# Kernel tuning notes

Measured on AMD Instinct MI355X. Metric: run time of the kernel, lower is better.

The kernel has to match this reference:

```python
import jax, jax.numpy as jnp
import numpy as np

N_NODES = 50000
N_EDGES = 800000
DIM = 128
N_LAYERS = 2          # num_layers - 1 GIN layers
NUM_GRAPHS = 512      # rows of the sparse graph_pool matrix
BN_EPS = 1e-5


def setup_inputs() -> dict:
    key = jax.random.key(0)
    ks = jax.random.split(key, 10)
    x = jax.random.normal(ks[0], (N_NODES, DIM), dtype=jnp.float32)
    edge_src = jax.random.randint(ks[1], (N_EDGES,), 0, N_NODES, dtype=jnp.int32)
    edge_dst = jax.random.randint(ks[2], (N_EDGES,), 0, N_NODES, dtype=jnp.int32)
    edge_weight = jax.random.uniform(ks[3], (N_EDGES,), dtype=jnp.float32)
    graph_ids = jnp.sort(jax.random.randint(ks[4], (N_NODES,), 0, NUM_GRAPHS, dtype=jnp.int32))
    pool_w = jnp.ones((N_NODES,), dtype=jnp.float32)
    scale = 1.0 / np.sqrt(DIM)
    W1 = jax.random.normal(ks[5], (N_LAYERS, DIM, DIM), dtype=jnp.float32) * scale
    b1 = jnp.zeros((N_LAYERS, DIM), dtype=jnp.float32)
    W2 = jax.random.normal(ks[6], (N_LAYERS, DIM, DIM), dtype=jnp.float32) * scale
    b2 = jnp.zeros((N_LAYERS, DIM), dtype=jnp.float32)
    bn_gamma = jnp.ones((N_LAYERS, DIM), dtype=jnp.float32)
    bn_beta = jnp.zeros((N_LAYERS, DIM), dtype=jnp.float32)
    return {"x": x, "edge_src": edge_src, "edge_dst": edge_dst,
            "edge_weight": edge_weight, "graph_ids": graph_ids, "pool_w": pool_w,
            "W1": W1, "b1": b1, "W2": W2, "b2": b2,
            "bn_gamma": bn_gamma, "bn_beta": bn_beta}


def reference(x, edge_src, edge_dst, edge_weight, graph_ids, pool_w,
              W1, b1, W2, b2, bn_gamma, bn_beta):
    h = x
    n = h.shape[0]
    for l in range(N_LAYERS):
        # pooled = adj @ h, adj in COO form: adj[dst, src] = edge_weight
        msg = edge_weight[:, None] * h[edge_src]                    # [E, D] gather
        pooled = jax.ops.segment_sum(msg, edge_dst, num_segments=n) # [N, D] scatter-add
        # 2-linear MLP (num_mlp_layers=2): Linear -> ReLU -> Linear
        hid = jax.nn.relu(pooled @ W1[l] + b1[l])
        z = hid @ W2[l] + b2[l]
        # BatchNorm1d over the node dimension (training-mode batch stats)
        mu = jnp.mean(z, axis=0)
        var = jnp.mean(jnp.square(z - mu), axis=0)
        z = bn_gamma[l] * (z - mu) * jax.lax.rsqrt(var + BN_EPS) + bn_beta[l]
        h = jax.nn.relu(z)
    x_nodes = h
    # pooled_x = graph_pool @ h, graph_pool[g, i] = pool_w[i] for node i in graph g
    pooled_x = jax.ops.segment_sum(pool_w[:, None] * h, graph_ids,
                                   num_segments=NUM_GRAPHS)
    return pooled_x, x_nodes
```

## Files before the change

kernel.cpp:

```cpp
#include <hip/hip_runtime.h>

#define N_NODES    50000
#define N_EDGES    800000
#define DIM        128
#define NUM_GRAPHS 512
#define BN_EPS     1e-5f

#define NBUCK      196
#define TILE       4096
#define MLP_ROWS   128
#define POOL_SPLIT 4

typedef unsigned int u32;
typedef unsigned short u16;
typedef __attribute__((ext_vector_type(8))) short bf16x8;
typedef __attribute__((ext_vector_type(4))) float f32x4;

__device__ __forceinline__ u16 f2bf(float f) {
    u32 u = __float_as_uint(f);
    u += 0x7FFF + ((u >> 16) & 1);
    return (u16)(u >> 16);
}
__device__ __forceinline__ float bf2f(u16 h) {
    return __uint_as_float((u32)h << 16);
}

__global__ __launch_bounds__(256)
void fill_zero2_kernel(float* __restrict__ p1, int n1, float* __restrict__ p2, int n2)
{
    int stride = gridDim.x * blockDim.x;
    for (int i = blockIdx.x * 256 + threadIdx.x; i < n1 + n2; i += stride) {
        if (i < n1) p1[i] = 0.f;
        else        p2[i - n1] = 0.f;
    }
}

__global__ __launch_bounds__(256)
void cvt_bf16_kernel(const float* __restrict__ in, u16* __restrict__ out, long long n4)
{
    long long stride = (long long)gridDim.x * blockDim.x;
    for (long long i = blockIdx.x * 256LL + threadIdx.x; i < n4; i += stride) {
        float4 v = ((const float4*)in)[i];
        ushort4 o;
        o.x = f2bf(v.x); o.y = f2bf(v.y); o.z = f2bf(v.z); o.w = f2bf(v.w);
        ((ushort4*)out)[i] = o;
    }
}

__global__ __launch_bounds__(256)
void cvt_wt_kernel(const float* __restrict__ W1, const float* __restrict__ W2,
                   u16* __restrict__ wt)
{
    int idx = blockIdx.x * 256 + threadIdx.x;
    if (idx >= 4 * 128 * 128) return;
    int m    = idx >> 14;
    int f    = idx & 16383;
    int c    = (f >> 11) & 7;
    int kk   = (f >> 9) & 3;
    int lane = (f >> 3) & 63;
    int e    = f & 7;
    int k = kk * 32 + ((lane >> 4) << 3) + e;
    int j = c * 16 + (lane & 15);
    const float* src = (m & 1) ? W2 : W1;
    src += (m >> 1) * 128 * 128;
    wt[idx] = f2bf(src[k * 128 + j]);
}

__global__ __launch_bounds__(256)
void bucket_hist(const int* __restrict__ dst, int* __restrict__ bucketCnt)
{
    __shared__ int cnt[NBUCK];
    int t = threadIdx.x;
    if (t < NBUCK) cnt[t] = 0;
    __syncthreads();
    int stride = gridDim.x * blockDim.x;
    for (int i = blockIdx.x * 256 + t; i < N_EDGES / 4; i += stride) {
        int4 d = ((const int4*)dst)[i];
        atomicAdd(&cnt[d.x >> 8], 1);
        atomicAdd(&cnt[d.y >> 8], 1);
        atomicAdd(&cnt[d.z >> 8], 1);
        atomicAdd(&cnt[d.w >> 8], 1);
    }
    __syncthreads();
    if (t < NBUCK && cnt[t] > 0) atomicAdd(&bucketCnt[t], cnt[t]);
}

__global__ __launch_bounds__(256)
void bucket_scan(const int* __restrict__ bucketCnt, int* __restrict__ bucketStart,
                 int* __restrict__ gCursor)
{
    __shared__ int s[256];
    int t = threadIdx.x;
    int v = (t < NBUCK) ? bucketCnt[t] : 0;
    s[t] = v;
    __syncthreads();
    for (int off = 1; off < 256; off <<= 1) {
        int x = (t >= off) ? s[t - off] : 0;
        __syncthreads();
        s[t] += x;
        __syncthreads();
    }
    int excl = s[t] - v;
    if (t <= NBUCK) bucketStart[t] = excl;
    if (t < NBUCK)  gCursor[t] = excl;
}

__global__ __launch_bounds__(512)
void partitionA(const int* __restrict__ src, const int* __restrict__ dst,
                const float* __restrict__ ew, int* __restrict__ gCursor,
                uint2* __restrict__ ed2)
{
    __shared__ int cnt[NBUCK];
    __shared__ int off[NBUCK];
    __shared__ int gb[NBUCK];
    __shared__ u32 stg_sw[TILE];
    __shared__ u32 stg_d[TILE];
    __shared__ int scanb[256];

    const int t = threadIdx.x;
    const int base = blockIdx.x * TILE;
    const int tcnt = min(TILE, N_EDGES - base);

    if (t < NBUCK) cnt[t] = 0;
    __syncthreads();

    u32 swv[8], dv[8];
    int rk[8], bk[8];
    #pragma unroll
    for (int j = 0; j < 8; ++j) {
        int e = base + j * 512 + t;
        if (e < N_EDGES) {
            int d = dst[e];
            swv[j] = ((u32)f2bf(ew[e]) << 16) | (u32)src[e];
            dv[j]  = (u32)d;
            bk[j]  = d >> 8;
            rk[j]  = atomicAdd(&cnt[bk[j]], 1);
        } else bk[j] = -1;
    }
    __syncthreads();

    {
        int v = (t < NBUCK) ? cnt[t] : 0;
        if (t < 256) scanb[t] = v;
        __syncthreads();
        for (int o = 1; o < 256; o <<= 1) {
            int x = (t < 256 && t >= o) ? scanb[t - o] : 0;
            __syncthreads();
            if (t < 256) scanb[t] += x;
            __syncthreads();
        }
        if (t < NBUCK) off[t] = scanb[t] - v;
    }
    __syncthreads();

    #pragma unroll
    for (int j = 0; j < 8; ++j) {
        if (bk[j] >= 0) {
            int idx = off[bk[j]] + rk[j];
            stg_sw[idx] = swv[j];
            stg_d[idx]  = dv[j];
        }
    }
    if (t < NBUCK && cnt[t] > 0) gb[t] = atomicAdd(&gCursor[t], cnt[t]);
    __syncthreads();

    for (int j = t; j < tcnt; j += 512) {
        u32 d = stg_d[j];
        int b = (int)(d >> 8);
        int pos = gb[b] + (j - off[b]);
        ed2[pos] = make_uint2(stg_sw[j], d);
    }
}

__global__ __launch_bounds__(256)
void partitionB(const uint2* __restrict__ ed2, const int* __restrict__ bucketStart,
                int* __restrict__ rowptr, u32* __restrict__ ed)
{
    __shared__ int hist[256];
    __shared__ int sc[256];
    __shared__ int cur[256];

    const int b = blockIdx.x;
    const int t = threadIdx.x;
    const int s = bucketStart[b];
    const int n = bucketStart[b + 1] - s;

    hist[t] = 0;
    __syncthreads();
    for (int j = t; j < n; j += 256)
        atomicAdd(&hist[ed2[s + j].y & 255u], 1);
    __syncthreads();

    int v = hist[t];
    sc[t] = v;
    __syncthreads();
    for (int o = 1; o < 256; o <<= 1) {
        int x = (t >= o) ? sc[t - o] : 0;
        __syncthreads();
        sc[t] += x;
        __syncthreads();
    }
    int excl = sc[t] - v;
    rowptr[b * 256 + t] = s + excl;
    cur[t] = s + excl;
    __syncthreads();

    for (int j = t; j < n; j += 256) {
        uint2 r = ed2[s + j];
        int d = (int)(r.y & 255u);
        int p = atomicAdd(&cur[d], 1);
        ed[p] = r.x;
    }
}

template<bool BN>
__global__ __launch_bounds__(256)
void gather_spmm(const u16* __restrict__ h, const u32* __restrict__ ed,
                 const int* __restrict__ rowptr, u16* __restrict__ pooled,
                 const float* __restrict__ stats, const float* __restrict__ gamma,
                 const float* __restrict__ beta)
{
    __shared__ float scs[128];
    __shared__ float shs[128];
    if (BN) {
        if (threadIdx.x < 128) {
            int c = threadIdx.x;
            float mu  = stats[c] * (1.f / N_NODES);
            float var = stats[128 + c] * (1.f / N_NODES) - mu * mu;
            float s   = gamma[c] * rsqrtf(var + BN_EPS);
            scs[c] = s;
            shs[c] = beta[c] - mu * s;
        }
        __syncthreads();
    }

    int node = blockIdx.x * 16 + (threadIdx.x >> 4);
    int lane = threadIdx.x & 15;
    int beg = rowptr[node];
    int end = rowptr[node + 1];

    float sc8[8], sh8[8];
    if (BN) {
        #pragma unroll
        for (int q = 0; q < 8; ++q) {
            sc8[q] = scs[lane * 8 + q];
            sh8[q] = shs[lane * 8 + q];
        }
    }

    float acc[8];
    #pragma unroll
    for (int q = 0; q < 8; ++q) acc[q] = 0.f;

    u32 sw_cur = (beg + lane < end) ? ed[beg + lane] : 0u;
    for (int base = beg; base < end; base += 16) {
        u32 sw_next = (base + 16 + lane < end) ? ed[base + 16 + lane] : 0u;
        int cnt = min(16, end - base);
        #pragma unroll 4
        for (int i = 0; i < cnt; ++i) {
            u32 rec = __shfl(sw_cur, i, 16);
            long long s = (long long)(rec & 0xFFFFu);
            float w = bf2f((u16)(rec >> 16));
            bf16x8 hv = *((const bf16x8*)(h + (s << 7)) + lane);
            #pragma unroll
            for (int q = 0; q < 8; ++q) {
                float v = bf2f((u16)hv[q]);
                if (BN) v = fmaxf(v * sc8[q] + sh8[q], 0.f);
                acc[q] += w * v;
            }
        }
        sw_cur = sw_next;
    }
    bf16x8 o;
    #pragma unroll
    for (int q = 0; q < 8; ++q) o[q] = (short)f2bf(acc[q]);
    *((bf16x8*)(pooled + ((long long)node << 7)) + lane) = o;
}

__global__ __launch_bounds__(512)
void fused_mlp(const u16* __restrict__ A, const u16* __restrict__ wtL,
               const float* __restrict__ b1, const float* __restrict__ b2,
               u16* __restrict__ Z, float* __restrict__ stats)
{
    __shared__ __align__(16) u16 wfrag[32768];
    __shared__ float ssum[128];
    __shared__ float ssq[128];

    const int tid  = threadIdx.x;
    const int lane = tid & 63;
    const int wave = tid >> 6;
    const int l15  = lane & 15;
    const int lk   = lane >> 4;
    const int row0 = blockIdx.x * MLP_ROWS;
    const int wrow = wave * 16;

    #pragma unroll
    for (int i = 0; i < 8; ++i) {
        int idx = tid + i * 512;
        *(bf16x8*)&wfrag[idx * 8] = *(const bf16x8*)(wtL + idx * 8);
    }
    if (tid < 128) { ssum[tid] = 0.f; ssq[tid] = 0.f; }

    bf16x8 afr[4];
    {
        int rg = row0 + wrow + l15;
        bool ok = rg < N_NODES;
        const u16* ap = A + (long long)rg * 128 + lk * 8;
        bf16x8 zero = {};
        #pragma unroll
        for (int kk = 0; kk < 4; ++kk)
            afr[kk] = ok ? *(const bf16x8*)(ap + kk * 32) : zero;
    }
    __syncthreads();

    f32x4 acc1[8];
    #pragma unroll
    for (int c = 0; c < 8; ++c) {
        float bv = b1[c * 16 + l15];
        f32x4 a = {bv, bv, bv, bv};
        #pragma unroll
        for (int kk = 0; kk < 4; ++kk) {
            bf16x8 w = *(bf16x8*)&wfrag[((c * 4 + kk) * 64 + lane) * 8];
            a = __builtin_amdgcn_mfma_f32_16x16x32_bf16(afr[kk], w, a, 0, 0, 0);
        }
        acc1[c] = a;
    }
    __syncthreads();

    #pragma unroll
    for (int c = 0; c < 8; ++c) {
        #pragma unroll
        for (int i = 0; i < 4; ++i) {
            int row = wrow + lk * 4 + i;
            int col = c * 16 + l15;
            wfrag[row * 128 + (col ^ ((row & 15) << 3))] = f2bf(fmaxf(acc1[c][i], 0.f));
        }
    }

    bf16x8 afr2[4];
    {
        int row = wrow + l15;
        #pragma unroll
        for (int kk = 0; kk < 4; ++kk)
            afr2[kk] = *(bf16x8*)&wfrag[row * 128 + ((kk * 32 + lk * 8) ^ ((row & 15) << 3))];
    }

    #pragma unroll
    for (int c = 0; c < 8; ++c) {
        float bv = b2[c * 16 + l15];
        f32x4 a = {bv, bv, bv, bv};
        #pragma unroll
        for (int kk = 0; kk < 4; ++kk) {
            bf16x8 w = *(bf16x8*)&wfrag[16384 + ((c * 4 + kk) * 64 + lane) * 8];
            a = __builtin_amdgcn_mfma_f32_16x16x32_bf16(afr2[kk], w, a, 0, 0, 0);
        }
        float s = 0.f, sq = 0.f;
        #pragma unroll
        for (int i = 0; i < 4; ++i) {
            int row = wrow + lk * 4 + i;
            int rg  = row0 + row;
            float v = a[i];
            bool ok = rg < N_NODES;
            if (ok) { s += v; sq += v * v; }
            wfrag[row * 128 + ((c * 16 + l15) ^ ((row & 15) << 3))] = ok ? f2bf(v) : (u16)0;
        }
        s  += __shfl_xor(s, 16);  s  += __shfl_xor(s, 32);
        sq += __shfl_xor(sq, 16); sq += __shfl_xor(sq, 32);
        if (lk == 0) {
            atomicAdd(&ssum[c * 16 + l15], s);
            atomicAdd(&ssq[c * 16 + l15], sq);
        }
    }

    #pragma unroll
    for (int j = 0; j < 4; ++j) {
        int chunk = j * 64 + lane;
        int rl  = chunk >> 4;
        int c8  = chunk & 15;
        int row = wrow + rl;
        int rg  = row0 + row;
        if (rg < N_NODES) {
            bf16x8 v = *(bf16x8*)&wfrag[row * 128 + ((c8 * 8) ^ ((row & 15) << 3))];
            *(bf16x8*)(Z + (long long)rg * 128 + c8 * 8) = v;
        }
    }
    __syncthreads();
    if (tid < 128) {
        atomicAdd(&stats[tid], ssum[tid]);
        atomicAdd(&stats[128 + tid], ssq[tid]);
    }
}

__global__ __launch_bounds__(256)
void graph_pool_bn(const u16* __restrict__ z, const float* __restrict__ stats,
                   const float* __restrict__ gamma, const float* __restrict__ beta,
                   const int* __restrict__ gid, const float* __restrict__ pw,
                   float* __restrict__ out_nodes, float* __restrict__ out_pool)
{
    __shared__ float scs[128];
    __shared__ float shs[128];
    if (threadIdx.x < 128) {
        int c = threadIdx.x;
        float mu  = stats[c] * (1.f / N_NODES);
        float var = stats[128 + c] * (1.f / N_NODES) - mu * mu;
        float s   = gamma[c] * rsqrtf(var + BN_EPS);
        scs[c] = s;
        shs[c] = beta[c] - mu * s;
    }
    __syncthreads();

    int g    = blockIdx.x >> 2;
    int part = blockIdx.x & 3;

    int lo = 0, hi = N_NODES;
    while (lo < hi) { int m = (lo + hi) >> 1; if (gid[m] < g) lo = m + 1; else hi = m; }
    int start = lo;
    hi = N_NODES;
    while (lo < hi) { int m = (lo + hi) >> 1; if (gid[m] < g + 1) lo = m + 1; else hi = m; }
    int end = lo;

    int len  = end - start;
    int qlen = (len + 3) >> 2;
    int s = start + part * qlen;
    int e = min(end, s + qlen);

    const int t  = threadIdx.x;
    const int rg = t >> 5;
    const int c4 = t & 31;
    float4 sc4 = *(float4*)&scs[c4 * 4];
    float4 sh4 = *(float4*)&shs[c4 * 4];

    float4 acc = make_float4(0.f, 0.f, 0.f, 0.f);
    for (int r = s + rg; r < e; r += 8) {
        float w = pw[r];
        ushort4 hv = *((const ushort4*)(z + (long long)r * DIM) + c4);
        float4 v;
        v.x = fmaxf(bf2f(hv.x) * sc4.x + sh4.x, 0.f);
        v.y = fmaxf(bf2f(hv.y) * sc4.y + sh4.y, 0.f);
        v.z = fmaxf(bf2f(hv.z) * sc4.z + sh4.z, 0.f);
        v.w = fmaxf(bf2f(hv.w) * sc4.w + sh4.w, 0.f);
        *((float4*)(out_nodes + (long long)r * DIM) + c4) = v;
        acc.x += w * v.x; acc.y += w * v.y;
        acc.z += w * v.z; acc.w += w * v.w;
    }

    __shared__ float4 sd[256];
    sd[t] = acc;
    __syncthreads();
    if (t < 32) {
        float4 tot = sd[t];
        #pragma unroll
        for (int i = 1; i < 8; ++i) {
            float4 v = sd[i * 32 + t];
            tot.x += v.x; tot.y += v.y; tot.z += v.z; tot.w += v.w;
        }
        float* op = out_pool + g * DIM + t * 4;
        atomicAdd(op + 0, tot.x);
        atomicAdd(op + 1, tot.y);
        atomicAdd(op + 2, tot.z);
        atomicAdd(op + 3, tot.w);
    }
}

extern "C" void kernel_launch(void* const* d_in, const int* in_sizes, int n_in,
                              void* d_out, int out_size, void* d_ws, size_t ws_size,
                              hipStream_t stream)
{
    const float* x    = (const float*)d_in[0];
    const int*   esrc = (const int*)d_in[1];
    const int*   edst = (const int*)d_in[2];
    const float* ew   = (const float*)d_in[3];
    const int*   gid  = (const int*)d_in[4];
    const float* pw   = (const float*)d_in[5];
    const float* W1   = (const float*)d_in[6];
    const float* b1   = (const float*)d_in[7];
    const float* W2   = (const float*)d_in[8];
    const float* b2   = (const float*)d_in[9];
    const float* gam  = (const float*)d_in[10];
    const float* bet  = (const float*)d_in[11];

    float* out_pool  = (float*)d_out;
    float* out_nodes = (float*)d_out + NUM_GRAPHS * DIM;

    const size_t NF = (size_t)N_NODES * DIM;
    char* w = (char*)d_ws;
    uint2* ed2      = (uint2*)w;      w += (size_t)N_EDGES * sizeof(uint2);
    u32*   ed       = (u32*)w;        w += (size_t)N_EDGES * sizeof(u32);
    u16*   pooledBf = (u16*)w;        w += NF * sizeof(u16);
    u16*   zBf      = (u16*)w;        w += NF * sizeof(u16);
    u16*   hx       = (u16*)w;        w += NF * sizeof(u16);
    u16*   wt       = (u16*)w;        w += (size_t)4 * 128 * 128 * sizeof(u16);
    float* stats0   = (float*)w;      w += 256 * sizeof(float);
    float* stats1   = (float*)w;      w += 256 * sizeof(float);
    int*   bucketCnt= (int*)w;        w += 256 * sizeof(int);
    int*   bucketStart=(int*)w;       w += 256 * sizeof(int);
    int*   gCursor  = (int*)w;        w += 256 * sizeof(int);
    int*   rowptr   = (int*)w;        w += (NBUCK * 256 + 64) * sizeof(int);

    const int mlpGrid    = (N_NODES + MLP_ROWS - 1) / MLP_ROWS;
    const int gatherGrid = (N_NODES + 15) / 16;
    const int partGrid   = (N_EDGES + TILE - 1) / TILE;

    fill_zero2_kernel<<<64, 256, 0, stream>>>(stats0, 768,
                                              out_pool, NUM_GRAPHS * DIM);
    bucket_hist<<<256, 256, 0, stream>>>(edst, bucketCnt);
    cvt_bf16_kernel<<<1024, 256, 0, stream>>>(x, hx, (long long)(NF / 4));
    cvt_wt_kernel<<<256, 256, 0, stream>>>(W1, W2, wt);
    bucket_scan<<<1, 256, 0, stream>>>(bucketCnt, bucketStart, gCursor);
    partitionA<<<partGrid, 512, 0, stream>>>(esrc, edst, ew, gCursor, ed2);
    partitionB<<<NBUCK, 256, 0, stream>>>(ed2, bucketStart, rowptr, ed);

    gather_spmm<false><<<gatherGrid, 256, 0, stream>>>(hx, ed, rowptr, pooledBf,
                                                       nullptr, nullptr, nullptr);
    fused_mlp<<<mlpGrid, 512, 0, stream>>>(pooledBf, wt, b1, b2, zBf, stats0);

    gather_spmm<true><<<gatherGrid, 256, 0, stream>>>(zBf, ed, rowptr, pooledBf,
                                                      stats0, gam, bet);
    fused_mlp<<<mlpGrid, 512, 0, stream>>>(pooledBf, wt + 32768,
                                           b1 + DIM, b2 + DIM, zBf, stats1);

    graph_pool_bn<<<NUM_GRAPHS * POOL_SPLIT, 256, 0, stream>>>(
        zBf, stats1, gam + DIM, bet + DIM, gid, pw, out_nodes, out_pool);
}
```

Measured before the change: 173.5 us.

## Fuse neighbor gather into MLP kernel and remove standalone scan/convert launches

The separate gather_spmm and fused_mlp kernels become one gather_mlp kernel. Each 512-thread block gathers its 128 node rows into a swizzled LDS tile and runs both MFMA layers on it, so the bf16 pooled buffer no longer goes to global memory and back. The bucket prefix scan is recomputed inside partitionA and partitionB instead of in a one-block kernel, and the x and weight bf16 conversions are merged into one launch. The price is much lower gather occupancy (about 96KB of LDS per block, 391 blocks) and uneven block tail balance, which could hurt the latency-bound gather.

```diff
diff --git a/kernel.cpp b/kernel.cpp
--- a/kernel.cpp
+++ b/kernel.cpp
@@ -36,34 +36,33 @@
 }
 
 __global__ __launch_bounds__(256)
-void cvt_bf16_kernel(const float* __restrict__ in, u16* __restrict__ out, long long n4)
-{
-    long long stride = (long long)gridDim.x * blockDim.x;
-    for (long long i = blockIdx.x * 256LL + threadIdx.x; i < n4; i += stride) {
-        float4 v = ((const float4*)in)[i];
-        ushort4 o;
-        o.x = f2bf(v.x); o.y = f2bf(v.y); o.z = f2bf(v.z); o.w = f2bf(v.w);
-        ((ushort4*)out)[i] = o;
-    }
-}
-
-__global__ __launch_bounds__(256)
-void cvt_wt_kernel(const float* __restrict__ W1, const float* __restrict__ W2,
-                   u16* __restrict__ wt)
-{
-    int idx = blockIdx.x * 256 + threadIdx.x;
-    if (idx >= 4 * 128 * 128) return;
-    int m    = idx >> 14;
-    int f    = idx & 16383;
-    int c    = (f >> 11) & 7;
-    int kk   = (f >> 9) & 3;
-    int lane = (f >> 3) & 63;
-    int e    = f & 7;
-    int k = kk * 32 + ((lane >> 4) << 3) + e;
-    int j = c * 16 + (lane & 15);
-    const float* src = (m & 1) ? W2 : W1;
-    src += (m >> 1) * 128 * 128;
-    wt[idx] = f2bf(src[k * 128 + j]);
+void cvt_all_kernel(const float* __restrict__ x, const float* __restrict__ W1,
+                    const float* __restrict__ W2, u16* __restrict__ hx,
+                    u16* __restrict__ wt)
+{
+    if (blockIdx.x < 256) {
+        int idx = blockIdx.x * 256 + threadIdx.x;
+        int m    = idx >> 14;
+        int f    = idx & 16383;
+        int c    = (f >> 11) & 7;
+        int kk   = (f >> 9) & 3;
+        int lane = (f >> 3) & 63;
+        int e    = f & 7;
+        int k = kk * 32 + ((lane >> 4) << 3) + e;
+        int j = c * 16 + (lane & 15);
+        const float* src = (m & 1) ? W2 : W1;
+        src += (m >> 1) * 128 * 128;
+        wt[idx] = f2bf(src[k * 128 + j]);
+    } else {
+        const long long n4 = (long long)N_NODES * DIM / 4;
+        long long stride = (long long)(gridDim.x - 256) * 256;
+        for (long long i = (blockIdx.x - 256) * 256LL + threadIdx.x; i < n4; i += stride) {
+            float4 v = ((const float4*)x)[i];
+            ushort4 o;
+            o.x = f2bf(v.x); o.y = f2bf(v.y); o.z = f2bf(v.z); o.w = f2bf(v.w);
+            ((ushort4*)hx)[i] = o;
+        }
+    }
 }
 
 __global__ __launch_bounds__(256)
@@ -85,31 +84,12 @@
     if (t < NBUCK && cnt[t] > 0) atomicAdd(&bucketCnt[t], cnt[t]);
 }
 
-__global__ __launch_bounds__(256)
-void bucket_scan(const int* __restrict__ bucketCnt, int* __restrict__ bucketStart,
-                 int* __restrict__ gCursor)
-{
-    __shared__ int s[256];
-    int t = threadIdx.x;
-    int v = (t < NBUCK) ? bucketCnt[t] : 0;
-    s[t] = v;
-    __syncthreads();
-    for (int off = 1; off < 256; off <<= 1) {
-        int x = (t >= off) ? s[t - off] : 0;
-        __syncthreads();
-        s[t] += x;
-        __syncthreads();
-    }
-    int excl = s[t] - v;
-    if (t <= NBUCK) bucketStart[t] = excl;
-    if (t < NBUCK)  gCursor[t] = excl;
-}
-
 __global__ __launch_bounds__(512)
 void partitionA(const int* __restrict__ src, const int* __restrict__ dst,
-                const float* __restrict__ ew, int* __restrict__ gCursor,
-                uint2* __restrict__ ed2)
-{
+                const float* __restrict__ ew, const int* __restrict__ bucketCnt,
+                int* __restrict__ gCursor, uint2* __restrict__ ed2)
+{
+    __shared__ int bstart[NBUCK];
     __shared__ int cnt[NBUCK];
     __shared__ int off[NBUCK];
     __shared__ int gb[NBUCK];
@@ -121,7 +101,18 @@
     const int base = blockIdx.x * TILE;
     const int tcnt = min(TILE, N_EDGES - base);
 
-    if (t < NBUCK) cnt[t] = 0;
+    {
+        int v = (t < NBUCK) ? bucketCnt[t] : 0;
+        if (t < 256) scanb[t] = v;
+        __syncthreads();
+        for (int o = 1; o < 256; o <<= 1) {
+            int x = (t < 256 && t >= o) ? scanb[t - o] : 0;
+            __syncthreads();
+            if (t < 256) scanb[t] += x;
+            __syncthreads();
+        }
+        if (t < NBUCK) { bstart[t] = scanb[t] - v; cnt[t] = 0; }
+    }
     __syncthreads();
 
     u32 swv[8], dv[8];
@@ -167,23 +158,39 @@
     for (int j = t; j < tcnt; j += 512) {
         u32 d = stg_d[j];
         int b = (int)(d >> 8);
-        int pos = gb[b] + (j - off[b]);
+        int pos = bstart[b] + gb[b] + (j - off[b]);
         ed2[pos] = make_uint2(stg_sw[j], d);
     }
 }
 
 __global__ __launch_bounds__(256)
-void partitionB(const uint2* __restrict__ ed2, const int* __restrict__ bucketStart,
+void partitionB(const uint2* __restrict__ ed2, const int* __restrict__ bucketCnt,
                 int* __restrict__ rowptr, u32* __restrict__ ed)
 {
+    __shared__ int bstart[256];
     __shared__ int hist[256];
     __shared__ int sc[256];
     __shared__ int cur[256];
 
     const int b = blockIdx.x;
     const int t = threadIdx.x;
-    const int s = bucketStart[b];
-    const int n = bucketStart[b + 1] - s;
+
+    {
+        int v = (t < NBUCK) ? bucketCnt[t] : 0;
+        sc[t] = v;
+        __syncthreads();
+        for (int o = 1; o < 256; o <<= 1) {
+            int x = (t >= o) ? sc[t - o] : 0;
+            __syncthreads();
+            sc[t] += x;
+            __syncthreads();
+        }
+        bstart[t] = sc[t] - v;
+    }
+    __syncthreads();
+
+    const int s = bstart[b];
+    const int n = bucketCnt[b];
 
     hist[t] = 0;
     __syncthreads();
@@ -214,77 +221,20 @@
 }
 
 template<bool BN>
-__global__ __launch_bounds__(256)
-void gather_spmm(const u16* __restrict__ h, const u32* __restrict__ ed,
-                 const int* __restrict__ rowptr, u16* __restrict__ pooled,
-                 const float* __restrict__ stats, const float* __restrict__ gamma,
-                 const float* __restrict__ beta)
-{
+__global__ __launch_bounds__(512)
+void gather_mlp(const u16* __restrict__ h, const u32* __restrict__ ed,
+                const int* __restrict__ rowptr, const u16* __restrict__ wtL,
+                const float* __restrict__ b1, const float* __restrict__ b2,
+                u16* __restrict__ Z, float* __restrict__ statsOut,
+                const float* __restrict__ statsIn, const float* __restrict__ gamma,
+                const float* __restrict__ beta)
+{
+    __shared__ __align__(16) u16 wfrag[32768];
+    __shared__ __align__(16) u16 pool[16384];
+    __shared__ float ssum[128];
+    __shared__ float ssq[128];
     __shared__ float scs[128];
     __shared__ float shs[128];
-    if (BN) {
-        if (threadIdx.x < 128) {
-            int c = threadIdx.x;
-            float mu  = stats[c] * (1.f / N_NODES);
-            float var = stats[128 + c] * (1.f / N_NODES) - mu * mu;
-            float s   = gamma[c] * rsqrtf(var + BN_EPS);
-            scs[c] = s;
-            shs[c] = beta[c] - mu * s;
-        }
-        __syncthreads();
-    }
-
-    int node = blockIdx.x * 16 + (threadIdx.x >> 4);
-    int lane = threadIdx.x & 15;
-    int beg = rowptr[node];
-    int end = rowptr[node + 1];
-
-    float sc8[8], sh8[8];
-    if (BN) {
-        #pragma unroll
-        for (int q = 0; q < 8; ++q) {
-            sc8[q] = scs[lane * 8 + q];
-            sh8[q] = shs[lane * 8 + q];
-        }
-    }
-
-    float acc[8];
-    #pragma unroll
-    for (int q = 0; q < 8; ++q) acc[q] = 0.f;
-
-    u32 sw_cur = (beg + lane < end) ? ed[beg + lane] : 0u;
-    for (int base = beg; base < end; base += 16) {
-        u32 sw_next = (base + 16 + lane < end) ? ed[base + 16 + lane] : 0u;
-        int cnt = min(16, end - base);
-        #pragma unroll 4
-        for (int i = 0; i < cnt; ++i) {
-            u32 rec = __shfl(sw_cur, i, 16);
-            long long s = (long long)(rec & 0xFFFFu);
-            float w = bf2f((u16)(rec >> 16));
-            bf16x8 hv = *((const bf16x8*)(h + (s << 7)) + lane);
-            #pragma unroll
-            for (int q = 0; q < 8; ++q) {
-                float v = bf2f((u16)hv[q]);
-                if (BN) v = fmaxf(v * sc8[q] + sh8[q], 0.f);
-                acc[q] += w * v;
-            }
-        }
-        sw_cur = sw_next;
-    }
-    bf16x8 o;
-    #pragma unroll
-    for (int q = 0; q < 8; ++q) o[q] = (short)f2bf(acc[q]);
-    *((bf16x8*)(pooled + ((long long)node << 7)) + lane) = o;
-}
-
-__global__ __launch_bounds__(512)
-void fused_mlp(const u16* __restrict__ A, const u16* __restrict__ wtL,
-               const float* __restrict__ b1, const float* __restrict__ b2,
-               u16* __restrict__ Z, float* __restrict__ stats)
-{
-    __shared__ __align__(16) u16 wfrag[32768];
-    __shared__ float ssum[128];
-    __shared__ float ssq[128];
 
     const int tid  = threadIdx.x;
     const int lane = tid & 63;
@@ -294,24 +244,81 @@
     const int row0 = blockIdx.x * MLP_ROWS;
     const int wrow = wave * 16;
 
-    #pragma unroll
-    for (int i = 0; i < 8; ++i) {
-        int idx = tid + i * 512;
-        *(bf16x8*)&wfrag[idx * 8] = *(const bf16x8*)(wtL + idx * 8);
-    }
     if (tid < 128) { ssum[tid] = 0.f; ssq[tid] = 0.f; }
+    if (BN) {
+        if (tid < 128) {
+            int c = tid;
+            float mu  = statsIn[c] * (1.f / N_NODES);
+            float var = statsIn[128 + c] * (1.f / N_NODES) - mu * mu;
+            float s   = gamma[c] * rsqrtf(var + BN_EPS);
+            scs[c] = s;
+            shs[c] = beta[c] - mu * s;
+        }
+        __syncthreads();
+    }
+
+    bf16x8 w8[8];
+    #pragma unroll
+    for (int i = 0; i < 8; ++i)
+        w8[i] = *(const bf16x8*)(wtL + (tid + i * 512) * 8);
+
+    const int grp = tid >> 4;
+    const int gl  = tid & 15;
+    float sc8[8], sh8[8];
+    if (BN) {
+        #pragma unroll
+        for (int q = 0; q < 8; ++q) {
+            sc8[q] = scs[gl * 8 + q];
+            sh8[q] = shs[gl * 8 + q];
+        }
+    }
+    #pragma unroll
+    for (int b = 0; b < 4; ++b) {
+        int r    = b * 32 + grp;
+        int node = row0 + r;
+        int beg = rowptr[node];
+        int end = rowptr[node + 1];
+        float acc[8];
+        #pragma unroll
+        for (int q = 0; q < 8; ++q) acc[q] = 0.f;
+
+        u32 sw_cur = (beg + gl < end) ? ed[beg + gl] : 0u;
+        for (int base = beg; base < end; base += 16) {
+            u32 sw_next = (base + 16 + gl < end) ? ed[base + 16 + gl] : 0u;
+            int cnt = min(16, end - base);
+            #pragma unroll 4
+            for (int i = 0; i < cnt; ++i) {
+                u32 rec = __shfl(sw_cur, i, 16);
+                long long s = (long long)(rec & 0xFFFFu);
+                float w = bf2f((u16)(rec >> 16));
+                bf16x8 hv = *((const bf16x8*)(h + (s << 7)) + gl);
+                #pragma unroll
+                for (int q = 0; q < 8; ++q) {
+                    float v = bf2f((u16)hv[q]);
+                    if (BN) v = fmaxf(v * sc8[q] + sh8[q], 0.f);
+                    acc[q] += w * v;
+                }
+            }
+            sw_cur = sw_next;
+        }
+        bf16x8 o;
+        #pragma unroll
+        for (int q = 0; q < 8; ++q) o[q] = (short)f2bf(acc[q]);
+        *(bf16x8*)&pool[r * 128 + ((gl * 8) ^ ((r & 15) << 3))] = o;
+    }
+
+    #pragma unroll
+    for (int i = 0; i < 8; ++i)
+        *(bf16x8*)&wfrag[(tid + i * 512) * 8] = w8[i];
+    __syncthreads();
 
     bf16x8 afr[4];
     {
-        int rg = row0 + wrow + l15;
-        bool ok = rg < N_NODES;
-        const u16* ap = A + (long long)rg * 128 + lk * 8;
-        bf16x8 zero = {};
+        int row = wrow + l15;
         #pragma unroll
         for (int kk = 0; kk < 4; ++kk)
-            afr[kk] = ok ? *(const bf16x8*)(ap + kk * 32) : zero;
-    }
-    __syncthreads();
+            afr[kk] = *(bf16x8*)&pool[row * 128 + ((kk * 32 + lk * 8) ^ ((row & 15) << 3))];
+    }
 
     f32x4 acc1[8];
     #pragma unroll
@@ -325,7 +332,6 @@
         }
         acc1[c] = a;
     }
-    __syncthreads();
 
     #pragma unroll
     for (int c = 0; c < 8; ++c) {
@@ -333,7 +339,7 @@
         for (int i = 0; i < 4; ++i) {
             int row = wrow + lk * 4 + i;
             int col = c * 16 + l15;
-            wfrag[row * 128 + (col ^ ((row & 15) << 3))] = f2bf(fmaxf(acc1[c][i], 0.f));
+            pool[row * 128 + (col ^ ((row & 15) << 3))] = f2bf(fmaxf(acc1[c][i], 0.f));
         }
     }
 
@@ -342,7 +348,7 @@
         int row = wrow + l15;
         #pragma unroll
         for (int kk = 0; kk < 4; ++kk)
-            afr2[kk] = *(bf16x8*)&wfrag[row * 128 + ((kk * 32 + lk * 8) ^ ((row & 15) << 3))];
+            afr2[kk] = *(bf16x8*)&pool[row * 128 + ((kk * 32 + lk * 8) ^ ((row & 15) << 3))];
     }
 
     #pragma unroll
@@ -362,7 +368,7 @@
             float v = a[i];
             bool ok = rg < N_NODES;
             if (ok) { s += v; sq += v * v; }
-            wfrag[row * 128 + ((c * 16 + l15) ^ ((row & 15) << 3))] = ok ? f2bf(v) : (u16)0;
+            pool[row * 128 + ((c * 16 + l15) ^ ((row & 15) << 3))] = ok ? f2bf(v) : (u16)0;
         }
         s  += __shfl_xor(s, 16);  s  += __shfl_xor(s, 32);
         sq += __shfl_xor(sq, 16); sq += __shfl_xor(sq, 32);
@@ -380,14 +386,14 @@
         int row = wrow + rl;
         int rg  = row0 + row;
         if (rg < N_NODES) {
-            bf16x8 v = *(bf16x8*)&wfrag[row * 128 + ((c8 * 8) ^ ((row & 15) << 3))];
+            bf16x8 v = *(bf16x8*)&pool[row * 128 + ((c8 * 8) ^ ((row & 15) << 3))];
             *(bf16x8*)(Z + (long long)rg * 128 + c8 * 8) = v;
         }
     }
     __syncthreads();
     if (tid < 128) {
-        atomicAdd(&stats[tid], ssum[tid]);
-        atomicAdd(&stats[128 + tid], ssq[tid]);
+        atomicAdd(&statsOut[tid], ssum[tid]);
+        atomicAdd(&statsOut[128 + tid], ssq[tid]);
     }
 }
 
@@ -486,39 +492,32 @@
     char* w = (char*)d_ws;
     uint2* ed2      = (uint2*)w;      w += (size_t)N_EDGES * sizeof(uint2);
     u32*   ed       = (u32*)w;        w += (size_t)N_EDGES * sizeof(u32);
-    u16*   pooledBf = (u16*)w;        w += NF * sizeof(u16);
     u16*   zBf      = (u16*)w;        w += NF * sizeof(u16);
     u16*   hx       = (u16*)w;        w += NF * sizeof(u16);
     u16*   wt       = (u16*)w;        w += (size_t)4 * 128 * 128 * sizeof(u16);
     float* stats0   = (float*)w;      w += 256 * sizeof(float);
     float* stats1   = (float*)w;      w += 256 * sizeof(float);
     int*   bucketCnt= (int*)w;        w += 256 * sizeof(int);
-    int*   bucketStart=(int*)w;       w += 256 * sizeof(int);
     int*   gCursor  = (int*)w;        w += 256 * sizeof(int);
     int*   rowptr   = (int*)w;        w += (NBUCK * 256 + 64) * sizeof(int);
 
-    const int mlpGrid    = (N_NODES + MLP_ROWS - 1) / MLP_ROWS;
-    const int gatherGrid = (N_NODES + 15) / 16;
-    const int partGrid   = (N_EDGES + TILE - 1) / TILE;
-
-    fill_zero2_kernel<<<64, 256, 0, stream>>>(stats0, 768,
+    const int mlpGrid  = (N_NODES + MLP_ROWS - 1) / MLP_ROWS;
+    const int partGrid = (N_EDGES + TILE - 1) / TILE;
+
+    fill_zero2_kernel<<<64, 256, 0, stream>>>(stats0, 1024,
                                               out_pool, NUM_GRAPHS * DIM);
     bucket_hist<<<256, 256, 0, stream>>>(edst, bucketCnt);
-    cvt_bf16_kernel<<<1024, 256, 0, stream>>>(x, hx, (long long)(NF / 4));
-    cvt_wt_kernel<<<256, 256, 0, stream>>>(W1, W2, wt);
-    bucket_scan<<<1, 256, 0, stream>>>(bucketCnt, bucketStart, gCursor);
-    partitionA<<<partGrid, 512, 0, stream>>>(esrc, edst, ew, gCursor, ed2);
-    partitionB<<<NBUCK, 256, 0, stream>>>(ed2, bucketStart, rowptr, ed);
-
-    gather_spmm<false><<<gatherGrid, 256, 0, stream>>>(hx, ed, rowptr, pooledBf,
-                                                       nullptr, nullptr, nullptr);
-    fused_mlp<<<mlpGrid, 512, 0, stream>>>(pooledBf, wt, b1, b2, zBf, stats0);
-
-    gather_spmm<true><<<gatherGrid, 256, 0, stream>>>(zBf, ed, rowptr, pooledBf,
-                                                      stats0, gam, bet);
-    fused_mlp<<<mlpGrid, 512, 0, stream>>>(pooledBf, wt + 32768,
-                                           b1 + DIM, b2 + DIM, zBf, stats1);
+    cvt_all_kernel<<<1280, 256, 0, stream>>>(x, W1, W2, hx, wt);
+    partitionA<<<partGrid, 512, 0, stream>>>(esrc, edst, ew, bucketCnt, gCursor, ed2);
+    partitionB<<<NBUCK, 256, 0, stream>>>(ed2, bucketCnt, rowptr, ed);
+
+    gather_mlp<false><<<mlpGrid, 512, 0, stream>>>(hx, ed, rowptr, wt,
+                                                   b1, b2, zBf, stats0,
+                                                   nullptr, nullptr, nullptr);
+    gather_mlp<true><<<mlpGrid, 512, 0, stream>>>(zBf, ed, rowptr, wt + 32768,
+                                                  b1 + DIM, b2 + DIM, hx, stats1,
+                                                  stats0, gam, bet);
 
     graph_pool_bn<<<NUM_GRAPHS * POOL_SPLIT, 256, 0, stream>>>(
-        zBf, stats1, gam + DIM, bet + DIM, gid, pw, out_nodes, out_pool);
-}
+        hx, stats1, gam + DIM, bet + DIM, gid, pw, out_nodes, out_pool);
+}
```

After: 249.9 us. 44.0% more time.

## Merge preprocessing kernels and fold bucket scan into partition kernels

Applied to the files above, without the earlier changes.

Combines the bf16 conversion of x, the weight repacking and the destination-bucket histogram into one multi-role prep kernel, chosen by block index. The single-block bucket_scan launch is removed: each partitionA and partitionB block recomputes the 196-entry prefix sum from bucketCnt in shared memory. gCursor is now zeroed by the fill kernel and used as a per-bucket offset relative to the recomputed bucket start. The aim is to cut three kernel launches and their serialization gaps, at the cost of a redundant small scan in every partition block.

```diff
diff --git a/kernel.cpp b/kernel.cpp
--- a/kernel.cpp
+++ b/kernel.cpp
@@ -36,80 +36,57 @@
 }
 
 __global__ __launch_bounds__(256)
-void cvt_bf16_kernel(const float* __restrict__ in, u16* __restrict__ out, long long n4)
-{
-    long long stride = (long long)gridDim.x * blockDim.x;
-    for (long long i = blockIdx.x * 256LL + threadIdx.x; i < n4; i += stride) {
-        float4 v = ((const float4*)in)[i];
-        ushort4 o;
-        o.x = f2bf(v.x); o.y = f2bf(v.y); o.z = f2bf(v.z); o.w = f2bf(v.w);
-        ((ushort4*)out)[i] = o;
-    }
-}
-
-__global__ __launch_bounds__(256)
-void cvt_wt_kernel(const float* __restrict__ W1, const float* __restrict__ W2,
-                   u16* __restrict__ wt)
-{
-    int idx = blockIdx.x * 256 + threadIdx.x;
-    if (idx >= 4 * 128 * 128) return;
-    int m    = idx >> 14;
-    int f    = idx & 16383;
-    int c    = (f >> 11) & 7;
-    int kk   = (f >> 9) & 3;
-    int lane = (f >> 3) & 63;
-    int e    = f & 7;
-    int k = kk * 32 + ((lane >> 4) << 3) + e;
-    int j = c * 16 + (lane & 15);
-    const float* src = (m & 1) ? W2 : W1;
-    src += (m >> 1) * 128 * 128;
-    wt[idx] = f2bf(src[k * 128 + j]);
-}
-
-__global__ __launch_bounds__(256)
-void bucket_hist(const int* __restrict__ dst, int* __restrict__ bucketCnt)
-{
-    __shared__ int cnt[NBUCK];
-    int t = threadIdx.x;
-    if (t < NBUCK) cnt[t] = 0;
-    __syncthreads();
-    int stride = gridDim.x * blockDim.x;
-    for (int i = blockIdx.x * 256 + t; i < N_EDGES / 4; i += stride) {
-        int4 d = ((const int4*)dst)[i];
-        atomicAdd(&cnt[d.x >> 8], 1);
-        atomicAdd(&cnt[d.y >> 8], 1);
-        atomicAdd(&cnt[d.z >> 8], 1);
-        atomicAdd(&cnt[d.w >> 8], 1);
-    }
-    __syncthreads();
-    if (t < NBUCK && cnt[t] > 0) atomicAdd(&bucketCnt[t], cnt[t]);
-}
-
-__global__ __launch_bounds__(256)
-void bucket_scan(const int* __restrict__ bucketCnt, int* __restrict__ bucketStart,
-                 int* __restrict__ gCursor)
-{
-    __shared__ int s[256];
-    int t = threadIdx.x;
-    int v = (t < NBUCK) ? bucketCnt[t] : 0;
-    s[t] = v;
-    __syncthreads();
-    for (int off = 1; off < 256; off <<= 1) {
-        int x = (t >= off) ? s[t - off] : 0;
-        __syncthreads();
-        s[t] += x;
-        __syncthreads();
-    }
-    int excl = s[t] - v;
-    if (t <= NBUCK) bucketStart[t] = excl;
-    if (t < NBUCK)  gCursor[t] = excl;
+void prep_kernel(const float* __restrict__ x, const float* __restrict__ W1,
+                 const float* __restrict__ W2, const int* __restrict__ dst,
+                 u16* __restrict__ hx, u16* __restrict__ wt,
+                 int* __restrict__ bucketCnt)
+{
+    if (blockIdx.x < 256) {
+        int idx = blockIdx.x * 256 + threadIdx.x;
+        int m    = idx >> 14;
+        int f    = idx & 16383;
+        int c    = (f >> 11) & 7;
+        int kk   = (f >> 9) & 3;
+        int lane = (f >> 3) & 63;
+        int e    = f & 7;
+        int k = kk * 32 + ((lane >> 4) << 3) + e;
+        int j = c * 16 + (lane & 15);
+        const float* src = (m & 1) ? W2 : W1;
+        src += (m >> 1) * 128 * 128;
+        wt[idx] = f2bf(src[k * 128 + j]);
+    } else if (blockIdx.x < 1280) {
+        const long long n4 = (long long)N_NODES * DIM / 4;
+        long long stride = 1024LL * 256;
+        for (long long i = (blockIdx.x - 256) * 256LL + threadIdx.x; i < n4; i += stride) {
+            float4 v = ((const float4*)x)[i];
+            ushort4 o;
+            o.x = f2bf(v.x); o.y = f2bf(v.y); o.z = f2bf(v.z); o.w = f2bf(v.w);
+            ((ushort4*)hx)[i] = o;
+        }
+    } else {
+        __shared__ int cnt[NBUCK];
+        int t = threadIdx.x;
+        if (t < NBUCK) cnt[t] = 0;
+        __syncthreads();
+        int stride = 256 * 256;
+        for (int i = (blockIdx.x - 1280) * 256 + t; i < N_EDGES / 4; i += stride) {
+            int4 d = ((const int4*)dst)[i];
+            atomicAdd(&cnt[d.x >> 8], 1);
+            atomicAdd(&cnt[d.y >> 8], 1);
+            atomicAdd(&cnt[d.z >> 8], 1);
+            atomicAdd(&cnt[d.w >> 8], 1);
+        }
+        __syncthreads();
+        if (t < NBUCK && cnt[t] > 0) atomicAdd(&bucketCnt[t], cnt[t]);
+    }
 }
 
 __global__ __launch_bounds__(512)
 void partitionA(const int* __restrict__ src, const int* __restrict__ dst,
-                const float* __restrict__ ew, int* __restrict__ gCursor,
-                uint2* __restrict__ ed2)
-{
+                const float* __restrict__ ew, const int* __restrict__ bucketCnt,
+                int* __restrict__ gCursor, uint2* __restrict__ ed2)
+{
+    __shared__ int bstart[NBUCK];
     __shared__ int cnt[NBUCK];
     __shared__ int off[NBUCK];
     __shared__ int gb[NBUCK];
@@ -121,7 +98,18 @@
     const int base = blockIdx.x * TILE;
     const int tcnt = min(TILE, N_EDGES - base);
 
-    if (t < NBUCK) cnt[t] = 0;
+    {
+        int v = (t < NBUCK) ? bucketCnt[t] : 0;
+        if (t < 256) scanb[t] = v;
+        __syncthreads();
+        for (int o = 1; o < 256; o <<= 1) {
+            int x = (t < 256 && t >= o) ? scanb[t - o] : 0;
+            __syncthreads();
+            if (t < 256) scanb[t] += x;
+            __syncthreads();
+        }
+        if (t < NBUCK) { bstart[t] = scanb[t] - v; cnt[t] = 0; }
+    }
     __syncthreads();
 
     u32 swv[8], dv[8];
@@ -167,23 +155,39 @@
     for (int j = t; j < tcnt; j += 512) {
         u32 d = stg_d[j];
         int b = (int)(d >> 8);
-        int pos = gb[b] + (j - off[b]);
+        int pos = bstart[b] + gb[b] + (j - off[b]);
         ed2[pos] = make_uint2(stg_sw[j], d);
     }
 }
 
 __global__ __launch_bounds__(256)
-void partitionB(const uint2* __restrict__ ed2, const int* __restrict__ bucketStart,
+void partitionB(const uint2* __restrict__ ed2, const int* __restrict__ bucketCnt,
                 int* __restrict__ rowptr, u32* __restrict__ ed)
 {
+    __shared__ int bstart[256];
     __shared__ int hist[256];
     __shared__ int sc[256];
     __shared__ int cur[256];
 
     const int b = blockIdx.x;
     const int t = threadIdx.x;
-    const int s = bucketStart[b];
-    const int n = bucketStart[b + 1] - s;
+
+    {
+        int v = (t < NBUCK) ? bucketCnt[t] : 0;
+        sc[t] = v;
+        __syncthreads();
+        for (int o = 1; o < 256; o <<= 1) {
+            int x = (t >= o) ? sc[t - o] : 0;
+            __syncthreads();
+            sc[t] += x;
+            __syncthreads();
+        }
+        bstart[t] = sc[t] - v;
+    }
+    __syncthreads();
+
+    const int s = bstart[b];
+    const int n = bucketCnt[b];
 
     hist[t] = 0;
     __syncthreads();
@@ -493,7 +497,6 @@
     float* stats0   = (float*)w;      w += 256 * sizeof(float);
     float* stats1   = (float*)w;      w += 256 * sizeof(float);
     int*   bucketCnt= (int*)w;        w += 256 * sizeof(int);
-    int*   bucketStart=(int*)w;       w += 256 * sizeof(int);
     int*   gCursor  = (int*)w;        w += 256 * sizeof(int);
     int*   rowptr   = (int*)w;        w += (NBUCK * 256 + 64) * sizeof(int);
 
@@ -501,14 +504,11 @@
     const int gatherGrid = (N_NODES + 15) / 16;
     const int partGrid   = (N_EDGES + TILE - 1) / TILE;
 
-    fill_zero2_kernel<<<64, 256, 0, stream>>>(stats0, 768,
+    fill_zero2_kernel<<<64, 256, 0, stream>>>(stats0, 1024,
                                               out_pool, NUM_GRAPHS * DIM);
-    bucket_hist<<<256, 256, 0, stream>>>(edst, bucketCnt);
-    cvt_bf16_kernel<<<1024, 256, 0, stream>>>(x, hx, (long long)(NF / 4));
-    cvt_wt_kernel<<<256, 256, 0, stream>>>(W1, W2, wt);
-    bucket_scan<<<1, 256, 0, stream>>>(bucketCnt, bucketStart, gCursor);
-    partitionA<<<partGrid, 512, 0, stream>>>(esrc, edst, ew, gCursor, ed2);
-    partitionB<<<NBUCK, 256, 0, stream>>>(ed2, bucketStart, rowptr, ed);
+    prep_kernel<<<1536, 256, 0, stream>>>(x, W1, W2, edst, hx, wt, bucketCnt);
+    partitionA<<<partGrid, 512, 0, stream>>>(esrc, edst, ew, bucketCnt, gCursor, ed2);
+    partitionB<<<NBUCK, 256, 0, stream>>>(ed2, bucketCnt, rowptr, ed);
 
     gather_spmm<false><<<gatherGrid, 256, 0, stream>>>(hx, ed, rowptr, pooledBf,
                                                        nullptr, nullptr, nullptr);
```

Result: faster. 166.4 us (-4.1%).
